# Kernel tuning notes

Hardware: AMD Instinct MI355X
Metric: run time of the kernel (lower is better)

The kernel has to match this reference:

```python
import jax, jax.numpy as jnp
import numpy as np

NUM_HEADS = 16
D_MODEL = 1024
HEAD_DIM = D_MODEL // NUM_HEADS
EPS = 1e-6


def setup_inputs() -> dict:
    key = jax.random.key(0)
    ks = jax.random.split(key, 9)
    B, S, D = 4, 8192, D_MODEL
    scale = 1.0 / np.sqrt(D)  # variance_scaling(1.0, fan_in, normal) approx
    inputs_q = jax.random.normal(ks[0], (B, S, D), dtype=jnp.float32)
    Wq = jax.random.normal(ks[1], (D, D), dtype=jnp.float32) * scale
    Wk = jax.random.normal(ks[2], (D, D), dtype=jnp.float32) * scale
    Wv = jax.random.normal(ks[3], (D, D), dtype=jnp.float32) * scale
    Wo = jax.random.normal(ks[4], (D, D), dtype=jnp.float32) * scale
    bq = jnp.zeros((D,), jnp.float32)
    bk = jnp.zeros((D,), jnp.float32)
    bv = jnp.zeros((D,), jnp.float32)
    bo = jnp.zeros((D,), jnp.float32)
    return {"inputs_q": inputs_q, "Wq": Wq, "bq": bq, "Wk": Wk, "bk": bk,
            "Wv": Wv, "bv": bv, "Wo": Wo, "bo": bo}


def _feature_map(x):
    return jax.nn.elu(x) + 1.0


def reference(inputs_q, Wq, bq, Wk, bk, Wv, bv, Wo, bo):
    B, S, D = inputs_q.shape
    H, Dh = NUM_HEADS, HEAD_DIM
    # QKV projections (self-attention: k,v inputs default to q input)
    q = (inputs_q @ Wq + bq).reshape(B, S, H, Dh)
    k = (inputs_q @ Wk + bk).reshape(B, S, H, Dh)
    v = (inputs_q @ Wv + bv).reshape(B, S, H, Dh)
    q = _feature_map(q)
    k = _feature_map(k)
    # KV outer-product accumulation: [B, H, Dh, Dh]
    kv = jnp.einsum('bkhd,bkhm->bhdm', k, v)
    out = jnp.einsum('bqhd,bhdm->bqhm', q, kv)
    # normalizer: q . sum_k(k)
    normalizer = jnp.einsum('bqhd,bkhd->bqh', q, k)
    normalizer = jnp.maximum(normalizer, EPS)
    out = out / normalizer[..., None]
    out = out.reshape(B, S, D)
    return out @ Wo + bo
```

## Files before the change

kernel.cpp:

```cpp
#include <hip/hip_runtime.h>
#include <cstdint>
#include <cstddef>

#define D_MODEL 1024
#define SEQ 8192

typedef __bf16  bf16x8 __attribute__((ext_vector_type(8)));
typedef short   short8 __attribute__((ext_vector_type(8)));
typedef float   f32x4  __attribute__((ext_vector_type(4)));
typedef unsigned short ushort_t;

__device__ __forceinline__ ushort_t f2bf(float f) {
  uint32_t u = __builtin_bit_cast(uint32_t, f);
  u += 0x7FFFu + ((u >> 16) & 1u);
  return (ushort_t)(u >> 16);
}
__device__ __forceinline__ float bf2f(ushort_t h) {
  return __builtin_bit_cast(float, (uint32_t)h << 16);
}
__device__ __forceinline__ void gll16(const void* g, void* l) {
  __builtin_amdgcn_global_load_lds(
      (const __attribute__((address_space(1))) void*)g,
      (__attribute__((address_space(3))) void*)l, 16, 0, 0);
}

__global__ void k_convert_x(const float* __restrict__ x, ushort_t* __restrict__ xb, int n) {
  int i = (blockIdx.x * 256 + threadIdx.x) * 8;
  if (i >= n) return;
  float4 v0 = *(const float4*)(x + i);
  float4 v1 = *(const float4*)(x + i + 4);
  ushort_t o[8] = { f2bf(v0.x), f2bf(v0.y), f2bf(v0.z), f2bf(v0.w),
                    f2bf(v1.x), f2bf(v1.y), f2bf(v1.z), f2bf(v1.w) };
  *(short8*)(xb + i) = *(const short8*)o;
}

__global__ void k_transpose_w(const float* W0, const float* W1, const float* W2, const float* W3,
                              ushort_t* T0, ushort_t* T1, ushort_t* T2, ushort_t* T3) {
  const float* src; ushort_t* dst;
  switch (blockIdx.z) {
    case 0: src = W0; dst = T0; break;
    case 1: src = W1; dst = T1; break;
    case 2: src = W2; dst = T2; break;
    default: src = W3; dst = T3; break;
  }
  __shared__ float tile[64][65];
  int tx = threadIdx.x;
  int c = tx & 63, r0 = tx >> 6;
  int bx = blockIdx.x * 64, by = blockIdx.y * 64;
  #pragma unroll
  for (int i = 0; i < 16; i++) {
    int r = i * 4 + r0;
    tile[r][c] = src[(size_t)(by + r) * D_MODEL + bx + c];
  }
  __syncthreads();
  #pragma unroll
  for (int i = 0; i < 16; i++) {
    int r = i * 4 + r0;
    dst[(size_t)(bx + r) * D_MODEL + by + c] = f2bf(tile[c][r]);
  }
}

template<int MODE>
__global__ __launch_bounds__(256) void k_gemm(const ushort_t* __restrict__ A,
                                              const ushort_t* __restrict__ Bt,
                                              const float* __restrict__ bias,
                                              ushort_t* __restrict__ outb,
                                              float* __restrict__ outf) {
  __shared__ __align__(16) ushort_t As[128 * 32];
  __shared__ __align__(16) ushort_t Bs[128 * 32];
  const int tid = threadIdx.x;
  const int ln = tid & 63;
  const int w = tid >> 6;
  const int wr = (w >> 1) * 64, wc = (w & 1) * 64;
  const int m0 = blockIdx.x * 128;
  const int n0 = blockIdx.y * 128;

  const int lr = tid >> 2;
  const int kg = (tid & 3) * 8;
  const ushort_t* gA0 = A + (size_t)(m0 + lr) * D_MODEL + kg;
  const ushort_t* gA1 = gA0 + (size_t)64 * D_MODEL;
  const ushort_t* gB0 = Bt + (size_t)(n0 + lr) * D_MODEL + kg;
  const ushort_t* gB1 = gB0 + (size_t)64 * D_MODEL;

  const int wb = __builtin_amdgcn_readfirstlane(w);
  ushort_t* lA0 = As + wb * 512;
  ushort_t* lA1 = As + 2048 + wb * 512;
  ushort_t* lB0 = Bs + wb * 512;
  ushort_t* lB1 = Bs + 2048 + wb * 512;

  f32x4 acc[4][4];
  #pragma unroll
  for (int i = 0; i < 4; i++)
    #pragma unroll
    for (int j = 0; j < 4; j++) acc[i][j] = (f32x4){0.f, 0.f, 0.f, 0.f};

  const int ar = ln & 15;
  const int aq = (ln >> 4) * 8;

  for (int kt = 0; kt < D_MODEL / 32; kt++) {
    gll16(gA0, lA0); gll16(gA1, lA1);
    gll16(gB0, lB0); gll16(gB1, lB1);
    gA0 += 32; gA1 += 32; gB0 += 32; gB1 += 32;
    __syncthreads();
    bf16x8 a[4], b[4];
    #pragma unroll
    for (int i = 0; i < 4; i++) a[i] = *(const bf16x8*)&As[(wr + i * 16 + ar) * 32 + aq];
    #pragma unroll
    for (int j = 0; j < 4; j++) b[j] = *(const bf16x8*)&Bs[(wc + j * 16 + ar) * 32 + aq];
    #pragma unroll
    for (int i = 0; i < 4; i++)
      #pragma unroll
      for (int j = 0; j < 4; j++)
        acc[i][j] = __builtin_amdgcn_mfma_f32_16x16x32_bf16(a[i], b[j], acc[i][j], 0, 0, 0);
    __syncthreads();
  }

  const int colb = ln & 15;
  const int rowb = (ln >> 4) * 4;
  #pragma unroll
  for (int j = 0; j < 4; j++) {
    int col = n0 + wc + j * 16 + colb;
    float bv = bias[col];
    #pragma unroll
    for (int i = 0; i < 4; i++) {
      int row = m0 + wr + i * 16 + rowb;
      #pragma unroll
      for (int r = 0; r < 4; r++) {
        float v = acc[i][j][r] + bv;
        if (MODE == 0) v = (v > 0.f) ? v + 1.f : __expf(v);
        if (MODE == 2) outf[(size_t)(row + r) * D_MODEL + col] = v;
        else           outb[(size_t)(row + r) * D_MODEL + col] = f2bf(v);
      }
    }
  }
}

__global__ __launch_bounds__(256) void k_kv_partial(const ushort_t* __restrict__ kmat,
                                                    const ushort_t* __restrict__ vmat,
                                                    float* __restrict__ part) {
  __shared__ __align__(16) ushort_t sbuf[4][2][2][512];
  const int tid = threadIdx.x, ln = tid & 63, w = tid >> 6;
  const int wb = __builtin_amdgcn_readfirstlane(w);
  const int bh = blockIdx.y, chunk = blockIdx.x;
  const int b = bh >> 4, h = bh & 15;
  const size_t cbase = ((size_t)b * SEQ + chunk * 1024 + w * 256) * D_MODEL + h * 64;
  const ushort_t* gk = kmat + cbase + (size_t)(ln >> 3) * D_MODEL + (ln & 7) * 8;
  const ushort_t* gv = vmat + cbase + (size_t)(ln >> 3) * D_MODEL + (ln & 7) * 8;

  float acc[8][8];
  float ksum[8];
  #pragma unroll
  for (int i = 0; i < 8; i++) { ksum[i] = 0.f;
    #pragma unroll
    for (int j = 0; j < 8; j++) acc[i][j] = 0.f; }

  const int r8 = (ln >> 3) * 8, c8 = (ln & 7) * 8;
  gll16(gk, &sbuf[wb][0][0][0]);
  gll16(gv, &sbuf[wb][0][1][0]);
  gk += 8 * D_MODEL; gv += 8 * D_MODEL;

  for (int bt = 0; bt < 32; bt++) {
    const int p = bt & 1;
    if (bt < 31) {
      gll16(gk, &sbuf[wb][p ^ 1][0][0]);
      gll16(gv, &sbuf[wb][p ^ 1][1][0]);
      gk += 8 * D_MODEL; gv += 8 * D_MODEL;
      __builtin_amdgcn_s_waitcnt(0x0F72);
    } else {
      __builtin_amdgcn_s_waitcnt(0x0F70);
    }
    #pragma unroll
    for (int s = 0; s < 8; s++) {
      short8 kk = *(const short8*)&sbuf[wb][p][0][s * 64 + r8];
      short8 vv = *(const short8*)&sbuf[wb][p][1][s * 64 + c8];
      float ka[8], va[8];
      #pragma unroll
      for (int i = 0; i < 8; i++) {
        ka[i] = __builtin_bit_cast(float, (uint32_t)(ushort_t)kk[i] << 16);
        va[i] = __builtin_bit_cast(float, (uint32_t)(ushort_t)vv[i] << 16);
      }
      #pragma unroll
      for (int i = 0; i < 8; i++) {
        ksum[i] += ka[i];
        #pragma unroll
        for (int j = 0; j < 8; j++) acc[i][j] += ka[i] * va[j];
      }
    }
  }
  float* p0 = part + ((size_t)bh * 32 + chunk * 4 + w) * 4160;
  #pragma unroll
  for (int i = 0; i < 8; i++)
    #pragma unroll
    for (int j = 0; j < 8; j++) p0[(r8 + i) * 64 + c8 + j] = acc[i][j];
  if ((ln & 7) == 0) {
    #pragma unroll
    for (int i = 0; i < 8; i++) p0[4096 + r8 + i] = ksum[i];
  }
}

__global__ void k_kv_reduce(const float* __restrict__ part, ushort_t* __restrict__ kvt) {
  const int bh = blockIdx.x, tid = threadIdx.x;
  const float* p0 = part + (size_t)bh * 32 * 4160;
  for (int idx = tid; idx < 4160; idx += 256) {
    float s = 0.f;
    #pragma unroll 4
    for (int c = 0; c < 32; c++) s += p0[(size_t)c * 4160 + idx];
    ushort_t bf = f2bf(s);
    if (idx < 4096) { int d = idx >> 6, m = idx & 63; kvt[(size_t)bh * 4160 + m * 64 + d] = bf; }
    else            { kvt[(size_t)bh * 4160 + 4096 + (idx - 4096)] = bf; }
  }
}

__global__ __launch_bounds__(256) void k_attn(const ushort_t* __restrict__ qmat,
                                              const ushort_t* __restrict__ kvt,
                                              ushort_t* __restrict__ attn) {
  __shared__ __align__(16) ushort_t kvs[65 * 80];
  __shared__ __align__(16) ushort_t qs[4][64 * 80];
  const int tid = threadIdx.x, ln = tid & 63, w = tid >> 6;
  const int bh = blockIdx.y, b = bh >> 4, h = bh & 15;

  for (int idx = tid; idx < 4160; idx += 256) {
    int m = idx >> 6, d = idx & 63;
    kvs[m * 80 + d] = kvt[(size_t)bh * 4160 + idx];
  }
  const size_t s0 = (size_t)b * SEQ + blockIdx.x * 256 + w * 64;
  #pragma unroll
  for (int c = 0; c < 8; c++) {
    int f = c * 64 + ln;
    int row = f >> 3, dg = (f & 7) * 8;
    short8 t = *(const short8*)&qmat[(s0 + row) * D_MODEL + h * 64 + dg];
    *(short8*)&qs[w][row * 80 + dg] = t;
  }
  __syncthreads();

  const int ar = ln & 15, aq = (ln >> 4) * 8;
  f32x4 acc[4][4], nacc[4];
  #pragma unroll
  for (int i = 0; i < 4; i++) { nacc[i] = (f32x4){0.f, 0.f, 0.f, 0.f};
    #pragma unroll
    for (int j = 0; j < 4; j++) acc[i][j] = (f32x4){0.f, 0.f, 0.f, 0.f}; }

  #pragma unroll
  for (int kk = 0; kk < 2; kk++) {
    const int ko = kk * 32 + aq;
    bf16x8 a[4], bb[4], bn;
    #pragma unroll
    for (int i = 0; i < 4; i++) a[i] = *(const bf16x8*)&qs[w][(i * 16 + ar) * 80 + ko];
    #pragma unroll
    for (int j = 0; j < 4; j++) bb[j] = *(const bf16x8*)&kvs[(j * 16 + ar) * 80 + ko];
    bn = *(const bf16x8*)&kvs[64 * 80 + ko];
    #pragma unroll
    for (int i = 0; i < 4; i++) {
      #pragma unroll
      for (int j = 0; j < 4; j++)
        acc[i][j] = __builtin_amdgcn_mfma_f32_16x16x32_bf16(a[i], bb[j], acc[i][j], 0, 0, 0);
      nacc[i] = __builtin_amdgcn_mfma_f32_16x16x32_bf16(a[i], bn, nacc[i], 0, 0, 0);
    }
  }

  const int colb = ln & 15, rowb = (ln >> 4) * 4;
  #pragma unroll
  for (int i = 0; i < 4; i++) {
    #pragma unroll
    for (int r = 0; r < 4; r++) {
      const int row = i * 16 + rowb + r;
      float nm = fmaxf(nacc[i][r], 1e-6f);
      float inv = 1.0f / nm;
      const size_t grow = s0 + row;
      #pragma unroll
      for (int j = 0; j < 4; j++) {
        float v = acc[i][j][r] * inv;
        attn[grow * D_MODEL + h * 64 + j * 16 + colb] = f2bf(v);
      }
    }
  }
}

extern "C" void kernel_launch(void* const* d_in, const int* in_sizes, int n_in,
                              void* d_out, int out_size, void* d_ws, size_t ws_size,
                              hipStream_t stream) {
  const float* x  = (const float*)d_in[0];
  const float* Wq = (const float*)d_in[1];
  const float* bq = (const float*)d_in[2];
  const float* Wk = (const float*)d_in[3];
  const float* bk = (const float*)d_in[4];
  const float* Wv = (const float*)d_in[5];
  const float* bv = (const float*)d_in[6];
  const float* Wo = (const float*)d_in[7];
  const float* bo = (const float*)d_in[8];
  float* out = (float*)d_out;

  const int M = in_sizes[0] / D_MODEL;
  const int B = M / SEQ;
  const int BH = B * 16;

  char* ws = (char*)d_ws;
  size_t off = 0;
  auto alloc = [&](size_t bytes) { char* p = ws + off; off += (bytes + 255) & ~(size_t)255; return p; };
  const size_t mb = (size_t)M * D_MODEL * 2;
  ushort_t* xb    = (ushort_t*)alloc(mb);
  ushort_t* qb    = (ushort_t*)alloc(mb);
  ushort_t* kb    = (ushort_t*)alloc(mb);
  ushort_t* vb    = (ushort_t*)alloc(mb);
  ushort_t* attnb = (ushort_t*)alloc(mb);
  ushort_t* wqt   = (ushort_t*)alloc((size_t)D_MODEL * D_MODEL * 2);
  ushort_t* wkt   = (ushort_t*)alloc((size_t)D_MODEL * D_MODEL * 2);
  ushort_t* wvt   = (ushort_t*)alloc((size_t)D_MODEL * D_MODEL * 2);
  ushort_t* wot   = (ushort_t*)alloc((size_t)D_MODEL * D_MODEL * 2);
  ushort_t* kvt   = (ushort_t*)alloc((size_t)BH * 4160 * 2);
  float*    part  = (float*)   alloc((size_t)BH * 32 * 4160 * 4);
  (void)ws_size; (void)n_in; (void)out_size;

  const int n = M * D_MODEL;
  k_convert_x<<<n / (256 * 8), 256, 0, stream>>>(x, xb, n);
  k_transpose_w<<<dim3(16, 16, 4), 256, 0, stream>>>(Wq, Wk, Wv, Wo, wqt, wkt, wvt, wot);

  dim3 gg(M / 128, 8);
  k_gemm<0><<<gg, 256, 0, stream>>>(xb, wqt, bq, qb, nullptr);
  k_gemm<0><<<gg, 256, 0, stream>>>(xb, wkt, bk, kb, nullptr);
  k_gemm<1><<<gg, 256, 0, stream>>>(xb, wvt, bv, vb, nullptr);

  k_kv_partial<<<dim3(8, BH), 256, 0, stream>>>(kb, vb, part);
  k_kv_reduce<<<BH, 256, 0, stream>>>(part, kvt);
  k_attn<<<dim3(SEQ / 256, BH), 256, 0, stream>>>(qb, kvt, attnb);

  k_gemm<2><<<gg, 256, 0, stream>>>(attnb, wot, bo, nullptr, out);
}
```

Baseline: 809.7 us.

## Fuse QKV projections into one GEMM with LDS-staged coalesced epilogue

Concatenates the transposed Wq, Wk and Wv into a single weight buffer and runs one GEMM launch over a 24-column-block grid, so one launch covers all three projections. The grid is linearized so consecutive blocks share the same A row tile, which should improve L2 reuse of the input. Epilogues now stage results in LDS (XOR-swizzled for bf16, padded for fp32) and write out with 16-byte coalesced stores instead of scattered 2- or 4-byte stores. The cost is extra LDS traffic, added barriers and a larger shared-memory footprint in the output GEMM.

```diff
diff --git a/kernel.cpp b/kernel.cpp
--- a/kernel.cpp
+++ b/kernel.cpp
@@ -14,9 +14,6 @@
   uint32_t u = __builtin_bit_cast(uint32_t, f);
   u += 0x7FFFu + ((u >> 16) & 1u);
   return (ushort_t)(u >> 16);
-}
-__device__ __forceinline__ float bf2f(ushort_t h) {
-  return __builtin_bit_cast(float, (uint32_t)h << 16);
 }
 __device__ __forceinline__ void gll16(const void* g, void* l) {
   __builtin_amdgcn_global_load_lds(
@@ -35,13 +32,13 @@
 }
 
 __global__ void k_transpose_w(const float* W0, const float* W1, const float* W2, const float* W3,
-                              ushort_t* T0, ushort_t* T1, ushort_t* T2, ushort_t* T3) {
+                              ushort_t* Tqkv, ushort_t* To) {
   const float* src; ushort_t* dst;
   switch (blockIdx.z) {
-    case 0: src = W0; dst = T0; break;
-    case 1: src = W1; dst = T1; break;
-    case 2: src = W2; dst = T2; break;
-    default: src = W3; dst = T3; break;
+    case 0: src = W0; dst = Tqkv; break;
+    case 1: src = W1; dst = Tqkv + (size_t)1024 * 1024; break;
+    case 2: src = W2; dst = Tqkv + (size_t)2048 * 1024; break;
+    default: src = W3; dst = To; break;
   }
   __shared__ float tile[64][65];
   int tx = threadIdx.x;
@@ -60,20 +57,31 @@
   }
 }
 
-template<int MODE>
+template<int MODE, int NY>
 __global__ __launch_bounds__(256) void k_gemm(const ushort_t* __restrict__ A,
                                               const ushort_t* __restrict__ Bt,
-                                              const float* __restrict__ bias,
-                                              ushort_t* __restrict__ outb,
+                                              const float* __restrict__ b0,
+                                              const float* __restrict__ b1,
+                                              const float* __restrict__ b2,
+                                              ushort_t* __restrict__ o0,
+                                              ushort_t* __restrict__ o1,
+                                              ushort_t* __restrict__ o2,
                                               float* __restrict__ outf) {
-  __shared__ __align__(16) ushort_t As[128 * 32];
-  __shared__ __align__(16) ushort_t Bs[128 * 32];
+  constexpr int SMEM_BYTES = (MODE == 2) ? 33792 : 32768;
+  __shared__ __align__(16) char smem[SMEM_BYTES];
+  ushort_t* As = (ushort_t*)smem;
+  ushort_t* Bs = (ushort_t*)(smem + 8192);
+
+  const int bid = blockIdx.x;
+  const int xb = bid / NY;
+  const int yb = bid % NY;
+  const int m0 = xb * 128;
+  const int n0 = yb * 128;
+
   const int tid = threadIdx.x;
   const int ln = tid & 63;
   const int w = tid >> 6;
   const int wr = (w >> 1) * 64, wc = (w & 1) * 64;
-  const int m0 = blockIdx.x * 128;
-  const int n0 = blockIdx.y * 128;
 
   const int lr = tid >> 2;
   const int kg = (tid & 3) * 8;
@@ -117,19 +125,65 @@
 
   const int colb = ln & 15;
   const int rowb = (ln >> 4) * 4;
-  #pragma unroll
-  for (int j = 0; j < 4; j++) {
-    int col = n0 + wc + j * 16 + colb;
-    float bv = bias[col];
-    #pragma unroll
-    for (int i = 0; i < 4; i++) {
-      int row = m0 + wr + i * 16 + rowb;
-      #pragma unroll
-      for (int r = 0; r < 4; r++) {
-        float v = acc[i][j][r] + bv;
-        if (MODE == 0) v = (v > 0.f) ? v + 1.f : __expf(v);
-        if (MODE == 2) outf[(size_t)(row + r) * D_MODEL + col] = v;
-        else           outb[(size_t)(row + r) * D_MODEL + col] = f2bf(v);
+
+  if (MODE == 0) {
+    const int region = yb >> 3;
+    const int nl0 = (yb & 7) * 128;
+    const float* bias = region == 0 ? b0 : (region == 1 ? b1 : b2);
+    ushort_t* gout    = region == 0 ? o0 : (region == 1 ? o1 : o2);
+    const bool act = region < 2;
+    ushort_t* Cs = (ushort_t*)smem;
+    #pragma unroll
+    for (int j = 0; j < 4; j++) {
+      const int col = wc + j * 16 + colb;
+      const float bv_ = bias[nl0 + col];
+      #pragma unroll
+      for (int i = 0; i < 4; i++) {
+        const int rbase = wr + i * 16 + rowb;
+        #pragma unroll
+        for (int r = 0; r < 4; r++) {
+          float v = acc[i][j][r] + bv_;
+          if (act) v = (v > 0.f) ? v + 1.f : __expf(v);
+          const int row = rbase + r;
+          const int cg = col >> 3, co = col & 7;
+          Cs[row * 128 + (((cg ^ (row & 15))) << 3) + co] = f2bf(v);
+        }
+      }
+    }
+    __syncthreads();
+    #pragma unroll
+    for (int c = 0; c < 8; c++) {
+      const int idx = c * 256 + tid;
+      const int row = idx >> 4, cg = idx & 15;
+      short8 t = *(const short8*)&Cs[row * 128 + ((cg ^ (row & 15)) << 3)];
+      *(short8*)&gout[(size_t)(m0 + row) * D_MODEL + nl0 + cg * 8] = t;
+    }
+  } else {
+    float* Cf = (float*)smem;
+    #pragma unroll
+    for (int h = 0; h < 2; h++) {
+      if (h) __syncthreads();
+      if ((wr >> 6) == h) {
+        #pragma unroll
+        for (int j = 0; j < 4; j++) {
+          const int col = wc + j * 16 + colb;
+          const float bv_ = b0[n0 + col];
+          #pragma unroll
+          for (int i = 0; i < 4; i++) {
+            const int rl = i * 16 + rowb;
+            #pragma unroll
+            for (int r = 0; r < 4; r++)
+              Cf[(rl + r) * 132 + col] = acc[i][j][r] + bv_;
+          }
+        }
+      }
+      __syncthreads();
+      #pragma unroll
+      for (int c = 0; c < 8; c++) {
+        const int idx = c * 256 + tid;
+        const int row = idx >> 5, cg = idx & 31;
+        float4 t = *(const float4*)&Cf[row * 132 + cg * 4];
+        *(float4*)&outf[(size_t)(m0 + h * 64 + row) * D_MODEL + n0 + cg * 4] = t;
       }
     }
   }
@@ -303,9 +357,7 @@
   ushort_t* kb    = (ushort_t*)alloc(mb);
   ushort_t* vb    = (ushort_t*)alloc(mb);
   ushort_t* attnb = (ushort_t*)alloc(mb);
-  ushort_t* wqt   = (ushort_t*)alloc((size_t)D_MODEL * D_MODEL * 2);
-  ushort_t* wkt   = (ushort_t*)alloc((size_t)D_MODEL * D_MODEL * 2);
-  ushort_t* wvt   = (ushort_t*)alloc((size_t)D_MODEL * D_MODEL * 2);
+  ushort_t* wqkvt = (ushort_t*)alloc((size_t)3 * D_MODEL * D_MODEL * 2);
   ushort_t* wot   = (ushort_t*)alloc((size_t)D_MODEL * D_MODEL * 2);
   ushort_t* kvt   = (ushort_t*)alloc((size_t)BH * 4160 * 2);
   float*    part  = (float*)   alloc((size_t)BH * 32 * 4160 * 4);
@@ -313,16 +365,13 @@
 
   const int n = M * D_MODEL;
   k_convert_x<<<n / (256 * 8), 256, 0, stream>>>(x, xb, n);
-  k_transpose_w<<<dim3(16, 16, 4), 256, 0, stream>>>(Wq, Wk, Wv, Wo, wqt, wkt, wvt, wot);
-
-  dim3 gg(M / 128, 8);
-  k_gemm<0><<<gg, 256, 0, stream>>>(xb, wqt, bq, qb, nullptr);
-  k_gemm<0><<<gg, 256, 0, stream>>>(xb, wkt, bk, kb, nullptr);
-  k_gemm<1><<<gg, 256, 0, stream>>>(xb, wvt, bv, vb, nullptr);
+  k_transpose_w<<<dim3(16, 16, 4), 256, 0, stream>>>(Wq, Wk, Wv, Wo, wqkvt, wot);
+
+  k_gemm<0, 24><<<(M / 128) * 24, 256, 0, stream>>>(xb, wqkvt, bq, bk, bv, qb, kb, vb, nullptr);
 
   k_kv_partial<<<dim3(8, BH), 256, 0, stream>>>(kb, vb, part);
   k_kv_reduce<<<BH, 256, 0, stream>>>(part, kvt);
   k_attn<<<dim3(SEQ / 256, BH), 256, 0, stream>>>(qb, kvt, attnb);
 
-  k_gemm<2><<<gg, 256, 0, stream>>>(attnb, wot, bo, nullptr, out);
-}
+  k_gemm<2, 8><<<(M / 128) * 8, 256, 0, stream>>>(attnb, wot, bo, nullptr, nullptr, nullptr, nullptr, nullptr, out);
+}
```

Result: faster. 751.9 us (-7.1%).
